# Kernel optimization log

Measured on AMD Instinct MI355X. Metric: run time of the kernel, lower is better.

The kernel has to match this reference:

```python
import jax, jax.numpy as jnp
import numpy as np

E4M3 = jnp.float8_e4m3fn  # forward fp8 dtype (HYBRID recipe fwd)

def fp8_qdq(x, fp8_dtype):
    # quantize (scale=1) to fp8 then dequantize back: models precision loss
    return x.astype(fp8_dtype).astype(x.dtype)

def setup_inputs() -> dict:
    key = jax.random.key(0)
    k1, k2 = jax.random.split(key)
    tokens, d_in, units = 4096, 1024, 4096
    x = jax.random.normal(k1, (tokens, d_in), dtype=jnp.float32)
    # kernel_initializer default: RandomNormal(mean=0.0, stddev=0.023)
    kernel = jax.random.normal(k2, (d_in, units), dtype=jnp.float32) * 0.023
    bias = jnp.zeros((units,), dtype=jnp.float32)
    return {"x": x, "kernel": kernel, "bias": bias}

def reference(x, kernel, bias):
    # fp8 quantize/dequantize prologue on activations and weights
    xq = fp8_qdq(x, E4M3)          # [tokens, d_in]
    kq = fp8_qdq(kernel, E4M3)     # [d_in, units]
    out = jnp.matmul(xq, kq) + bias  # [tokens, units]
    # gelu approximate=True (tanh approximation)
    return jax.nn.gelu(out, approximate=True)
```

## Files before the change

kernel.cpp:

```cpp
#include <hip/hip_runtime.h>
#include <hip/hip_bf16.h>

typedef float f32x4 __attribute__((ext_vector_type(4)));
typedef long  l2    __attribute__((ext_vector_type(2)));

__device__ __forceinline__ void gld16(const void* g, void* l) {
    __builtin_amdgcn_global_load_lds(
        (const __attribute__((address_space(1))) void*)g,
        (__attribute__((address_space(3))) void*)l,
        16, 0, 0);
}

__device__ __forceinline__ float gelu_tanh(float x) {
    float u = 0.7978845608028654f * x * (1.0f + 0.044715f * x * x);
    float e = __expf(2.0f * u);
    float t = 1.0f - 2.0f / (e + 1.0f);
    return 0.5f * x * (1.0f + t);
}


__global__ __launch_bounds__(256) void quant_fused_kernel(
        const float* __restrict__ x,  unsigned char* __restrict__ Aq,
        const float* __restrict__ w,  unsigned char* __restrict__ BTq,
        int nA, int K, int N) {
    __shared__ unsigned char lds[64 * 68];
    const int tid = threadIdx.x;

    if (blockIdx.x < nA) {
        int i = blockIdx.x * 256 + tid;
        float4 v = reinterpret_cast<const float4*>(x)[i];
        int pk = 0;
        pk = __builtin_amdgcn_cvt_pk_fp8_f32(v.x, v.y, pk, false);
        pk = __builtin_amdgcn_cvt_pk_fp8_f32(v.z, v.w, pk, true);
        const long k4 = (long)i * 4;
        const int  row = (int)(k4 / K);
        const int  k   = (int)(k4 % K);
        const int  o   = k & 63;
        const int  g   = (o & 31) >> 3;
        const int  s   = (o & 7) + ((o >> 5) & 1) * 8;
        const int  c   = g ^ ((row >> 1) & 3);
        *reinterpret_cast<unsigned int*>(
            Aq + (long)row * K + (k & ~63) + (c << 4) + s) = (unsigned int)pk;
        return;
    }

    const int bid = blockIdx.x - nA;
    const int n0 = (bid & (N / 64 - 1)) * 64;
    const int k0 = (bid / (N / 64)) * 64;

    #pragma unroll
    for (int p = 0; p < 4; ++p) {
        int s = p * 256 + tid;
        int r = s >> 4;
        int c = s & 15;
        float4 v = *reinterpret_cast<const float4*>(
            w + (long)(k0 + r) * N + n0 + c * 4);
        int pk = 0;
        pk = __builtin_amdgcn_cvt_pk_fp8_f32(v.x, v.y, pk, false);
        pk = __builtin_amdgcn_cvt_pk_fp8_f32(v.z, v.w, pk, true);
        *reinterpret_cast<unsigned int*>(&lds[r * 68 + c * 4]) = (unsigned int)pk;
    }
    __syncthreads();
    #pragma unroll
    for (int p = 0; p < 4; ++p) {
        int sidx = p * 256 + tid;
        int n  = sidx >> 4;
        int kg = sidx & 15;
        unsigned int wv = 0;
        #pragma unroll
        for (int j = 0; j < 4; ++j)
            wv |= (unsigned int)lds[(kg * 4 + j) * 68 + n] << (8 * j);
        const int nn = n0 + n;
        const int o  = kg * 4;
        const int g  = (o & 31) >> 3;
        const int s  = (o & 7) + ((o >> 5) & 1) * 8;
        const int c  = g ^ ((nn >> 1) & 3);
        *reinterpret_cast<unsigned int*>(
            BTq + (long)nn * K + k0 + (c << 4) + s) = wv;
    }
}

__global__ __launch_bounds__(512, 8) void gemm_fp8_kernel(
        const unsigned char* __restrict__ A,
        const unsigned char* __restrict__ BT,
        const float* __restrict__ bias,
        float* __restrict__ out,
        int M, int N, int K) {
    constexpr int BM = 128, BN = 128, BK = 64;
    __shared__ union {
        unsigned char buf[2][(BM + BN) * BK];
        float ep[8][1088];
    } sm;

    const int tid  = threadIdx.x;
    const int lane = tid & 63;
    const int wid  = tid >> 6;
    const int wm   = wid >> 1;
    const int wn   = wid & 1;

    const int bid = blockIdx.x;
    const int xcd = bid & 7, idx = bid >> 3;
    const int tile_m = (xcd >> 1) * 8  + (idx & 7);
    const int tile_n = (xcd & 1) * 16 + (idx >> 3);
    const int m0 = tile_m * BM, n0 = tile_n * BN;

    const int lrow = lane & 15;
    const int kgrp = lane >> 4;
    const int chunkoff = ((kgrp ^ ((lrow >> 1) & 3)) << 4);

    const int srow   = tid >> 2;
    const int schunk = (tid & 3) << 4;
    const unsigned char* gA = A  + (long)(m0 + srow) * K + schunk;
    const unsigned char* gB = BT + (long)(n0 + srow) * K + schunk;

    const int aBase = (wm * 32 + lrow) * 64 + chunkoff;
    const int bBase = 8192 + (wn * 64 + lrow) * 64 + chunkoff;

    f32x4 acc[2][4] = {};

    const int NT = K / BK;

#define STAGE_A(BB, TT)                                                   \
    gld16(gA + (long)(TT) * BK, &sm.buf[BB][wid * 1024])
#define STAGE_B(BB, TT)                                                   \
    gld16(gB + (long)(TT) * BK, &sm.buf[BB][8192 + wid * 1024])

#define MFMA_Q(BJ0, BR)                                                   \
    _Pragma("unroll") for (int ks = 0; ks < 2; ++ks)                      \
    _Pragma("unroll") for (int fi = 0; fi < 2; ++fi)                      \
    _Pragma("unroll") for (int fj = 0; fj < 2; ++fj)                      \
        acc[fi][(BJ0) + fj] = __builtin_amdgcn_mfma_f32_16x16x32_fp8_fp8( \
            a01[fi][ks], BR[fj][ks], acc[fi][(BJ0) + fj], 0, 0, 0)

    STAGE_A(0, 0); STAGE_B(0, 0);
    asm volatile("s_waitcnt vmcnt(0)" ::: "memory");
    __builtin_amdgcn_s_barrier();

    for (int t = 0; t < NT; ++t) {
        const int cur = t & 1, nxt = cur ^ 1;
        const unsigned char* sL = &sm.buf[cur][0];
        const bool st = (t + 1 < NT);
        l2 a01[2], b01[2], b23[2];

        if (st) { STAGE_A(nxt, t + 1); }
        #pragma unroll
        for (int f = 0; f < 2; ++f) {
            a01[f] = *reinterpret_cast<const l2*>(sL + aBase + f * 1024);
            b01[f] = *reinterpret_cast<const l2*>(sL + bBase + f * 1024);
        }
        __builtin_amdgcn_s_barrier();
        asm volatile("s_waitcnt lgkmcnt(0)" ::: "memory");
        __builtin_amdgcn_sched_barrier(0);
        __builtin_amdgcn_s_setprio(1);
        MFMA_Q(0, b01);
        __builtin_amdgcn_s_setprio(0);

        if (st) { STAGE_B(nxt, t + 1); }
        #pragma unroll
        for (int f = 0; f < 2; ++f)
            b23[f] = *reinterpret_cast<const l2*>(sL + bBase + 2048 + f * 1024);
        __builtin_amdgcn_s_barrier();
        asm volatile("s_waitcnt lgkmcnt(0)" ::: "memory");
        __builtin_amdgcn_sched_barrier(0);
        __builtin_amdgcn_s_setprio(1);
        MFMA_Q(2, b23);
        __builtin_amdgcn_s_setprio(0);
        __builtin_amdgcn_sched_barrier(0);

        if (t < NT - 1) {
            asm volatile("s_waitcnt vmcnt(0)" ::: "memory");
            __builtin_amdgcn_sched_barrier(0);
            __builtin_amdgcn_s_barrier();
        }
    }

    __syncthreads();
    float* eplds = sm.ep[wid];
    const int  col0   = n0 + wn * 64;
    const long rbase0 = m0 + wm * 32;
    float bv[4];
    #pragma unroll
    for (int bj = 0; bj < 4; ++bj) bv[bj] = bias[col0 + bj * 16 + lrow];

    #pragma unroll
    for (int ai = 0; ai < 2; ++ai) {
        #pragma unroll
        for (int bj = 0; bj < 4; ++bj) {
            #pragma unroll
            for (int r = 0; r < 4; ++r) {
                float xv = acc[ai][bj][r] + bv[bj];
                eplds[(kgrp * 4 + r) * 68 + bj * 16 + lrow] = gelu_tanh(xv);
            }
        }
        #pragma unroll
        for (int s = 0; s < 4; ++s) {
            f32x4 v = *reinterpret_cast<const f32x4*>(
                eplds + (s * 4 + kgrp) * 68 + lrow * 4);
            __builtin_nontemporal_store(v, reinterpret_cast<f32x4*>(
                out + (rbase0 + ai * 16 + s * 4 + kgrp) * N + col0 + lrow * 4));
        }
    }
#undef STAGE_A
#undef STAGE_B
#undef MFMA_Q
}

extern "C" void kernel_launch(void* const* d_in, const int* in_sizes, int n_in,
                              void* d_out, int out_size, void* d_ws, size_t ws_size,
                              hipStream_t stream) {
    const float* x    = (const float*)d_in[0];
    const float* w    = (const float*)d_in[1];
    const float* bias = (const float*)d_in[2];
    float* out = (float*)d_out;

    const int units  = in_sizes[2];
    const int dmodel = in_sizes[1] / units;
    const int tokens = in_sizes[0] / dmodel;

    unsigned char* Aq  = (unsigned char*)d_ws;
    unsigned char* BTq = Aq + (size_t)tokens * dmodel;

    const int nA = tokens * dmodel / 4 / 256;
    const int nB = (units / 64) * (dmodel / 64);
    quant_fused_kernel<<<dim3(nA + nB), dim3(256), 0, stream>>>(
        x, Aq, w, BTq, nA, dmodel, units);

    const int nblocks = (tokens / 128) * (units / 128);
    gemm_fp8_kernel<<<dim3(nblocks), dim3(512), 0, stream>>>(
        Aq, BTq, bias, out, tokens, units, dmodel);
}
```

Measured before the change: 48.19 us.

## Process two N-tiles per block, overlapping epilogue with next tile's loads

Each GEMM block now computes two adjacent 128-column output tiles in sequence, halving the grid. The operand loads for the second tile are issued before the first tile's GELU epilogue runs, so global loads overlap the epilogue math and stores. The LDS-staged epilogue is replaced by direct scalar nontemporal stores, which frees the shared-memory union. The cost is less coalesced 4-byte stores, a smaller grid with fewer blocks to balance across CUs, and some fragile hand-placed vmcnt waits.

```diff
diff --git a/kernel.cpp b/kernel.cpp
--- a/kernel.cpp
+++ b/kernel.cpp
@@ -87,10 +87,7 @@
         float* __restrict__ out,
         int M, int N, int K) {
     constexpr int BM = 128, BN = 128, BK = 64;
-    __shared__ union {
-        unsigned char buf[2][(BM + BN) * BK];
-        float ep[8][1088];
-    } sm;
+    __shared__ unsigned char buf[2][(BM + BN) * BK];
 
     const int tid  = threadIdx.x;
     const int lane = tid & 63;
@@ -100,9 +97,9 @@
 
     const int bid = blockIdx.x;
     const int xcd = bid & 7, idx = bid >> 3;
-    const int tile_m = (xcd >> 1) * 8  + (idx & 7);
-    const int tile_n = (xcd & 1) * 16 + (idx >> 3);
-    const int m0 = tile_m * BM, n0 = tile_n * BN;
+    const int tile_m = (xcd >> 1) * 8 + (idx & 7);
+    const int pcol   = (xcd & 1) * 8 + (idx >> 3);
+    const int m0 = tile_m * BM;
 
     const int lrow = lane & 15;
     const int kgrp = lane >> 4;
@@ -110,20 +107,19 @@
 
     const int srow   = tid >> 2;
     const int schunk = (tid & 3) << 4;
-    const unsigned char* gA = A  + (long)(m0 + srow) * K + schunk;
-    const unsigned char* gB = BT + (long)(n0 + srow) * K + schunk;
+    const unsigned char* gA  = A  + (long)(m0 + srow) * K + schunk;
+    const unsigned char* gB0 = BT + (long)(pcol * 256 + srow) * K + schunk;
+    const unsigned char* gB1 = gB0 + (long)128 * K;
 
     const int aBase = (wm * 32 + lrow) * 64 + chunkoff;
     const int bBase = 8192 + (wn * 64 + lrow) * 64 + chunkoff;
 
-    f32x4 acc[2][4] = {};
-
     const int NT = K / BK;
 
 #define STAGE_A(BB, TT)                                                   \
-    gld16(gA + (long)(TT) * BK, &sm.buf[BB][wid * 1024])
-#define STAGE_B(BB, TT)                                                   \
-    gld16(gB + (long)(TT) * BK, &sm.buf[BB][8192 + wid * 1024])
+    gld16(gA + (long)(TT) * BK, &buf[BB][wid * 1024])
+#define STAGE_B(BB, GB, TT)                                               \
+    gld16((GB) + (long)(TT) * BK, &buf[BB][8192 + wid * 1024])
 
 #define MFMA_Q(BJ0, BR)                                                   \
     _Pragma("unroll") for (int ks = 0; ks < 2; ++ks)                      \
@@ -132,72 +128,85 @@
         acc[fi][(BJ0) + fj] = __builtin_amdgcn_mfma_f32_16x16x32_fp8_fp8( \
             a01[fi][ks], BR[fj][ks], acc[fi][(BJ0) + fj], 0, 0, 0)
 
-    STAGE_A(0, 0); STAGE_B(0, 0);
-    asm volatile("s_waitcnt vmcnt(0)" ::: "memory");
-    __builtin_amdgcn_s_barrier();
-
-    for (int t = 0; t < NT; ++t) {
-        const int cur = t & 1, nxt = cur ^ 1;
-        const unsigned char* sL = &sm.buf[cur][0];
-        const bool st = (t + 1 < NT);
-        l2 a01[2], b01[2], b23[2];
-
-        if (st) { STAGE_A(nxt, t + 1); }
+    #pragma unroll
+    for (int rep = 0; rep < 2; ++rep) {
+        const unsigned char* gB = rep ? gB1 : gB0;
+
+        if (rep == 0) {
+            STAGE_A(0, 0); STAGE_B(0, gB, 0);
+            asm volatile("s_waitcnt vmcnt(0)" ::: "memory");
+            __builtin_amdgcn_s_barrier();
+        }
+
+        f32x4 acc[2][4] = {};
+
+        for (int t = 0; t < NT; ++t) {
+            const int cur = t & 1, nxt = cur ^ 1;
+            const unsigned char* sL = &buf[cur][0];
+            const bool stg = (t + 1 < NT) && !(rep == 1 && t == 0);
+            l2 a01[2], b01[2], b23[2];
+
+            if (stg) { STAGE_A(nxt, t + 1); }
+            #pragma unroll
+            for (int f = 0; f < 2; ++f) {
+                a01[f] = *reinterpret_cast<const l2*>(sL + aBase + f * 1024);
+                b01[f] = *reinterpret_cast<const l2*>(sL + bBase + f * 1024);
+            }
+            __builtin_amdgcn_s_barrier();
+            asm volatile("s_waitcnt lgkmcnt(0)" ::: "memory");
+            __builtin_amdgcn_sched_barrier(0);
+            __builtin_amdgcn_s_setprio(1);
+            MFMA_Q(0, b01);
+            __builtin_amdgcn_s_setprio(0);
+
+            if (stg) { STAGE_B(nxt, gB, t + 1); }
+            #pragma unroll
+            for (int f = 0; f < 2; ++f)
+                b23[f] = *reinterpret_cast<const l2*>(sL + bBase + 2048 + f * 1024);
+            __builtin_amdgcn_s_barrier();
+            asm volatile("s_waitcnt lgkmcnt(0)" ::: "memory");
+            __builtin_amdgcn_sched_barrier(0);
+            __builtin_amdgcn_s_setprio(1);
+            MFMA_Q(2, b23);
+            __builtin_amdgcn_s_setprio(0);
+            __builtin_amdgcn_sched_barrier(0);
+
+            if (t < NT - 1) {
+                if (stg) { asm volatile("s_waitcnt vmcnt(0)" ::: "memory"); }
+                __builtin_amdgcn_sched_barrier(0);
+                __builtin_amdgcn_s_barrier();
+            }
+        }
+
+        const int col0 = pcol * 256 + rep * 128 + wn * 64 + lrow;
+        float* po = out + (long)(m0 + wm * 32 + kgrp * 4) * N + col0;
+        float bv[4];
         #pragma unroll
-        for (int f = 0; f < 2; ++f) {
-            a01[f] = *reinterpret_cast<const l2*>(sL + aBase + f * 1024);
-            b01[f] = *reinterpret_cast<const l2*>(sL + bBase + f * 1024);
-        }
-        __builtin_amdgcn_s_barrier();
-        asm volatile("s_waitcnt lgkmcnt(0)" ::: "memory");
-        __builtin_amdgcn_sched_barrier(0);
-        __builtin_amdgcn_s_setprio(1);
-        MFMA_Q(0, b01);
-        __builtin_amdgcn_s_setprio(0);
-
-        if (st) { STAGE_B(nxt, t + 1); }
+        for (int bj = 0; bj < 4; ++bj) bv[bj] = bias[col0 + bj * 16];
+
+        if (rep == 0) {
+            __builtin_amdgcn_s_barrier();
+            STAGE_A(0, 0); STAGE_B(0, gB1, 0);
+            STAGE_A(1, 1); STAGE_B(1, gB1, 1);
+            __builtin_amdgcn_sched_barrier(0);
+        }
+
         #pragma unroll
-        for (int f = 0; f < 2; ++f)
-            b23[f] = *reinterpret_cast<const l2*>(sL + bBase + 2048 + f * 1024);
-        __builtin_amdgcn_s_barrier();
-        asm volatile("s_waitcnt lgkmcnt(0)" ::: "memory");
-        __builtin_amdgcn_sched_barrier(0);
-        __builtin_amdgcn_s_setprio(1);
-        MFMA_Q(2, b23);
-        __builtin_amdgcn_s_setprio(0);
-        __builtin_amdgcn_sched_barrier(0);
-
-        if (t < NT - 1) {
-            asm volatile("s_waitcnt vmcnt(0)" ::: "memory");
-            __builtin_amdgcn_sched_barrier(0);
-            __builtin_amdgcn_s_barrier();
-        }
-    }
-
-    __syncthreads();
-    float* eplds = sm.ep[wid];
-    const int  col0   = n0 + wn * 64;
-    const long rbase0 = m0 + wm * 32;
-    float bv[4];
-    #pragma unroll
-    for (int bj = 0; bj < 4; ++bj) bv[bj] = bias[col0 + bj * 16 + lrow];
-
-    #pragma unroll
-    for (int ai = 0; ai < 2; ++ai) {
-        #pragma unroll
-        for (int bj = 0; bj < 4; ++bj) {
+        for (int ai = 0; ai < 2; ++ai)
             #pragma unroll
-            for (int r = 0; r < 4; ++r) {
-                float xv = acc[ai][bj][r] + bv[bj];
-                eplds[(kgrp * 4 + r) * 68 + bj * 16 + lrow] = gelu_tanh(xv);
-            }
-        }
-        #pragma unroll
-        for (int s = 0; s < 4; ++s) {
-            f32x4 v = *reinterpret_cast<const f32x4*>(
-                eplds + (s * 4 + kgrp) * 68 + lrow * 4);
-            __builtin_nontemporal_store(v, reinterpret_cast<f32x4*>(
-                out + (rbase0 + ai * 16 + s * 4 + kgrp) * N + col0 + lrow * 4));
+            for (int bj = 0; bj < 4; ++bj)
+                #pragma unroll
+                for (int r = 0; r < 4; ++r) {
+                    float xv = acc[ai][bj][r] + bv[bj];
+                    __builtin_nontemporal_store(gelu_tanh(xv),
+                        po + (long)(ai * 16 + r) * N + bj * 16);
+                }
+
+        if (rep == 0) {
+            __builtin_amdgcn_sched_barrier(0);
+            asm volatile("s_waitcnt vmcnt(32)" ::: "memory");
+            __builtin_amdgcn_sched_barrier(0);
+            __builtin_amdgcn_s_barrier();
         }
     }
 #undef STAGE_A
@@ -225,7 +234,7 @@
     quant_fused_kernel<<<dim3(nA + nB), dim3(256), 0, stream>>>(
         x, Aq, w, BTq, nA, dmodel, units);
 
-    const int nblocks = (tokens / 128) * (units / 128);
-    gemm_fp8_kernel<<<dim3(nblocks), dim3(512), 0, stream>>>(
+    const int npairs = (tokens / 128) * (units / 256);
+    gemm_fp8_kernel<<<dim3(npairs), dim3(512), 0, stream>>>(
         Aq, BTq, bias, out, tokens, units, dmodel);
 }
```

Measured after the change: 64.48 us. 33.8% more time.

## Switch GEMM to 32x32x64 scaled fp8 MFMA with matching operand layout

Applied to the files above, without the earlier changes.

Replaces the 16x16x32 fp8 MFMA tiles with the gfx950 mfma_scale 32x32x64 f8f6f4 instruction, using unit scales. The quantization kernel now writes A and B^T in a simple XOR-swizzled 16-byte chunk layout that matches the new operand fragments. The main loop issues both A and B stage loads together and uses one barrier phase per k-step instead of two. The epilogue is rewritten for the 32x32 accumulator layout through a padded LDS transpose. The aim is fewer MFMA and LDS instructions and less synchronisation, at the cost of larger accumulators, a lower occupancy hint, and unaligned 16-byte LDS reads in the epilogue.

```diff
diff --git a/kernel.cpp b/kernel.cpp
--- a/kernel.cpp
+++ b/kernel.cpp
@@ -1,8 +1,10 @@
 #include <hip/hip_runtime.h>
 #include <hip/hip_bf16.h>
 
-typedef float f32x4 __attribute__((ext_vector_type(4)));
-typedef long  l2    __attribute__((ext_vector_type(2)));
+typedef float f32x4  __attribute__((ext_vector_type(4)));
+typedef float f32x16 __attribute__((ext_vector_type(16)));
+typedef int   i32x4  __attribute__((ext_vector_type(4)));
+typedef int   i32x8  __attribute__((ext_vector_type(8)));
 
 __device__ __forceinline__ void gld16(const void* g, void* l) {
     __builtin_amdgcn_global_load_lds(
@@ -36,11 +38,9 @@
         const int  row = (int)(k4 / K);
         const int  k   = (int)(k4 % K);
         const int  o   = k & 63;
-        const int  g   = (o & 31) >> 3;
-        const int  s   = (o & 7) + ((o >> 5) & 1) * 8;
-        const int  c   = g ^ ((row >> 1) & 3);
+        const int  c   = (o >> 4) ^ ((row >> 1) & 3);
         *reinterpret_cast<unsigned int*>(
-            Aq + (long)row * K + (k & ~63) + (c << 4) + s) = (unsigned int)pk;
+            Aq + (long)row * K + (k & ~63) + (c << 4) + (o & 15)) = (unsigned int)pk;
         return;
     }
 
@@ -71,16 +71,13 @@
         for (int j = 0; j < 4; ++j)
             wv |= (unsigned int)lds[(kg * 4 + j) * 68 + n] << (8 * j);
         const int nn = n0 + n;
-        const int o  = kg * 4;
-        const int g  = (o & 31) >> 3;
-        const int s  = (o & 7) + ((o >> 5) & 1) * 8;
-        const int c  = g ^ ((nn >> 1) & 3);
+        const int c  = (kg >> 2) ^ ((nn >> 1) & 3);
         *reinterpret_cast<unsigned int*>(
-            BTq + (long)nn * K + k0 + (c << 4) + s) = wv;
-    }
-}
-
-__global__ __launch_bounds__(512, 8) void gemm_fp8_kernel(
+            BTq + (long)nn * K + k0 + (c << 4) + ((kg & 3) * 4)) = wv;
+    }
+}
+
+__global__ __launch_bounds__(512, 4) void gemm_fp8_kernel(
         const unsigned char* __restrict__ A,
         const unsigned char* __restrict__ BT,
         const float* __restrict__ bias,
@@ -89,7 +86,7 @@
     constexpr int BM = 128, BN = 128, BK = 64;
     __shared__ union {
         unsigned char buf[2][(BM + BN) * BK];
-        float ep[8][1088];
+        float ep[8][1056];
     } sm;
 
     const int tid  = threadIdx.x;
@@ -104,19 +101,30 @@
     const int tile_n = (xcd & 1) * 16 + (idx >> 3);
     const int m0 = tile_m * BM, n0 = tile_n * BN;
 
-    const int lrow = lane & 15;
-    const int kgrp = lane >> 4;
-    const int chunkoff = ((kgrp ^ ((lrow >> 1) & 3)) << 4);
+    const int l31 = lane & 31;
+    const int h   = lane >> 5;
 
     const int srow   = tid >> 2;
     const int schunk = (tid & 3) << 4;
     const unsigned char* gA = A  + (long)(m0 + srow) * K + schunk;
     const unsigned char* gB = BT + (long)(n0 + srow) * K + schunk;
 
-    const int aBase = (wm * 32 + lrow) * 64 + chunkoff;
-    const int bBase = 8192 + (wn * 64 + lrow) * 64 + chunkoff;
-
-    f32x4 acc[2][4] = {};
+    const int rA = wm * 32 + l31;
+    const int xA = (rA >> 1) & 3;
+    int offA[2], offB[2][2];
+    #pragma unroll
+    for (int q = 0; q < 2; ++q)
+        offA[q] = rA * 64 + ((((h << 1) | q) ^ xA) << 4);
+    #pragma unroll
+    for (int fj = 0; fj < 2; ++fj) {
+        const int rB = wn * 64 + fj * 32 + l31;
+        const int xB = (rB >> 1) & 3;
+        #pragma unroll
+        for (int q = 0; q < 2; ++q)
+            offB[fj][q] = 8192 + rB * 64 + ((((h << 1) | q) ^ xB) << 4);
+    }
+
+    f32x16 acc0 = {}, acc1 = {};
 
     const int NT = K / BK;
 
@@ -125,13 +133,6 @@
 #define STAGE_B(BB, TT)                                                   \
     gld16(gB + (long)(TT) * BK, &sm.buf[BB][8192 + wid * 1024])
 
-#define MFMA_Q(BJ0, BR)                                                   \
-    _Pragma("unroll") for (int ks = 0; ks < 2; ++ks)                      \
-    _Pragma("unroll") for (int fi = 0; fi < 2; ++fi)                      \
-    _Pragma("unroll") for (int fj = 0; fj < 2; ++fj)                      \
-        acc[fi][(BJ0) + fj] = __builtin_amdgcn_mfma_f32_16x16x32_fp8_fp8( \
-            a01[fi][ks], BR[fj][ks], acc[fi][(BJ0) + fj], 0, 0, 0)
-
     STAGE_A(0, 0); STAGE_B(0, 0);
     asm volatile("s_waitcnt vmcnt(0)" ::: "memory");
     __builtin_amdgcn_s_barrier();
@@ -139,31 +140,30 @@
     for (int t = 0; t < NT; ++t) {
         const int cur = t & 1, nxt = cur ^ 1;
         const unsigned char* sL = &sm.buf[cur][0];
-        const bool st = (t + 1 < NT);
-        l2 a01[2], b01[2], b23[2];
-
-        if (st) { STAGE_A(nxt, t + 1); }
-        #pragma unroll
-        for (int f = 0; f < 2; ++f) {
-            a01[f] = *reinterpret_cast<const l2*>(sL + aBase + f * 1024);
-            b01[f] = *reinterpret_cast<const l2*>(sL + bBase + f * 1024);
-        }
+        const bool stg = (t + 1 < NT);
+
+        if (stg) { STAGE_A(nxt, t + 1); STAGE_B(nxt, t + 1); }
+
+        i32x4 alo = *reinterpret_cast<const i32x4*>(sL + offA[0]);
+        i32x4 ahi = *reinterpret_cast<const i32x4*>(sL + offA[1]);
+        i32x4 b0lo = *reinterpret_cast<const i32x4*>(sL + offB[0][0]);
+        i32x4 b0hi = *reinterpret_cast<const i32x4*>(sL + offB[0][1]);
+        i32x4 b1lo = *reinterpret_cast<const i32x4*>(sL + offB[1][0]);
+        i32x4 b1hi = *reinterpret_cast<const i32x4*>(sL + offB[1][1]);
+
         __builtin_amdgcn_s_barrier();
         asm volatile("s_waitcnt lgkmcnt(0)" ::: "memory");
         __builtin_amdgcn_sched_barrier(0);
+
+        i32x8 av = __builtin_shufflevector(alo, ahi, 0, 1, 2, 3, 4, 5, 6, 7);
+        i32x8 b0 = __builtin_shufflevector(b0lo, b0hi, 0, 1, 2, 3, 4, 5, 6, 7);
+        i32x8 b1 = __builtin_shufflevector(b1lo, b1hi, 0, 1, 2, 3, 4, 5, 6, 7);
+
         __builtin_amdgcn_s_setprio(1);
-        MFMA_Q(0, b01);
-        __builtin_amdgcn_s_setprio(0);
-
-        if (st) { STAGE_B(nxt, t + 1); }
-        #pragma unroll
-        for (int f = 0; f < 2; ++f)
-            b23[f] = *reinterpret_cast<const l2*>(sL + bBase + 2048 + f * 1024);
-        __builtin_amdgcn_s_barrier();
-        asm volatile("s_waitcnt lgkmcnt(0)" ::: "memory");
-        __builtin_amdgcn_sched_barrier(0);
-        __builtin_amdgcn_s_setprio(1);
-        MFMA_Q(2, b23);
+        acc0 = __builtin_amdgcn_mfma_scale_f32_32x32x64_f8f6f4(
+            av, b0, acc0, 0, 0, 0, 127, 0, 127);
+        acc1 = __builtin_amdgcn_mfma_scale_f32_32x32x64_f8f6f4(
+            av, b1, acc1, 0, 0, 0, 127, 0, 127);
         __builtin_amdgcn_s_setprio(0);
         __builtin_amdgcn_sched_barrier(0);
 
@@ -176,33 +176,36 @@
 
     __syncthreads();
     float* eplds = sm.ep[wid];
-    const int  col0   = n0 + wn * 64;
     const long rbase0 = m0 + wm * 32;
-    float bv[4];
-    #pragma unroll
-    for (int bj = 0; bj < 4; ++bj) bv[bj] = bias[col0 + bj * 16 + lrow];
-
-    #pragma unroll
-    for (int ai = 0; ai < 2; ++ai) {
-        #pragma unroll
-        for (int bj = 0; bj < 4; ++bj) {
-            #pragma unroll
-            for (int r = 0; r < 4; ++r) {
-                float xv = acc[ai][bj][r] + bv[bj];
-                eplds[(kgrp * 4 + r) * 68 + bj * 16 + lrow] = gelu_tanh(xv);
-            }
-        }
-        #pragma unroll
-        for (int s = 0; s < 4; ++s) {
-            f32x4 v = *reinterpret_cast<const f32x4*>(
-                eplds + (s * 4 + kgrp) * 68 + lrow * 4);
-            __builtin_nontemporal_store(v, reinterpret_cast<f32x4*>(
-                out + (rbase0 + ai * 16 + s * 4 + kgrp) * N + col0 + lrow * 4));
-        }
-    }
+
+#define EPI(ACC, FJ)                                                      \
+    do {                                                                  \
+        const int colb = n0 + wn * 64 + (FJ) * 32;                        \
+        const float bv = bias[colb + l31];                                \
+        _Pragma("unroll")                                                 \
+        for (int r = 0; r < 16; ++r) {                                    \
+            const int row = (r & 3) + 8 * (r >> 2) + 4 * h;               \
+            eplds[row * 33 + l31] = gelu_tanh(ACC[r] + bv);               \
+        }                                                                 \
+        asm volatile("s_waitcnt lgkmcnt(0)" ::: "memory");                \
+        __builtin_amdgcn_s_barrier();                                     \
+        _Pragma("unroll")                                                 \
+        for (int ps = 0; ps < 4; ++ps) {                                  \
+            const int rr = ps * 8 + (lane >> 3);                          \
+            f32x4 v = *reinterpret_cast<const f32x4*>(                    \
+                eplds + rr * 33 + (lane & 7) * 4);                        \
+            __builtin_nontemporal_store(v, reinterpret_cast<f32x4*>(      \
+                out + (rbase0 + rr) * N + colb + (lane & 7) * 4));        \
+        }                                                                 \
+        asm volatile("s_waitcnt lgkmcnt(0)" ::: "memory");                \
+        __builtin_amdgcn_s_barrier();                                     \
+    } while (0)
+
+    EPI(acc0, 0);
+    EPI(acc1, 1);
 #undef STAGE_A
 #undef STAGE_B
-#undef MFMA_Q
+#undef EPI
 }
 
 extern "C" void kernel_launch(void* const* d_in, const int* in_sizes, int n_in,
```

Measured after the change: 50.25 us. 1.04x slower.
